# Kernel tuning notes

Measured on AMD Instinct MI355X. Metric: run time of the kernel, lower is better.

The kernel has to match this reference:

```python
import jax, jax.numpy as jnp
import numpy as np

N_NODES = 100000
N_EDGES = 1600000
HID = 128


def setup_inputs() -> dict:
    key = jax.random.key(0)
    ks = jax.random.split(key, 16)

    def w(k, fan_in, fan_out, scale=None):
        s = scale if scale is not None else 1.0 / np.sqrt(fan_in)
        return (jax.random.normal(k, (fan_in, fan_out), jnp.float32) * s)

    inp = {
        "h": jax.random.normal(ks[0], (N_NODES, HID), jnp.float32),
        "edge_index": jax.random.randint(ks[1], (2, N_EDGES), 0, N_NODES, jnp.int64),
        "x": jax.random.normal(ks[2], (N_NODES, 3), jnp.float32),
        "v": jax.random.normal(ks[3], (N_NODES, 3), jnp.float32),
        # edge_mlp: Linear(257,128) -> ReLU -> Linear(128,128) -> ReLU
        "we1": w(ks[4], 2 * HID + 1, HID), "be1": jnp.zeros((HID,), jnp.float32),
        "we2": w(ks[5], HID, HID), "be2": jnp.zeros((HID,), jnp.float32),
        # node_mlp: Linear(384,128) -> ReLU -> Linear(128,128)
        "wn1": w(ks[6], 3 * HID, HID), "bn1": jnp.zeros((HID,), jnp.float32),
        "wn2": w(ks[7], HID, HID), "bn2": jnp.zeros((HID,), jnp.float32),
        # coord_mlp_vel: Linear(128,128) -> ReLU -> Linear(128,1)
        "wv1": w(ks[8], HID, HID), "bv1": jnp.zeros((HID,), jnp.float32),
        "wv2": w(ks[9], HID, 1), "bv2": jnp.zeros((1,), jnp.float32),
        # coord_mlp: Linear(128,128) -> ReLU -> Linear(128,1, bias=False, xavier gain 0.001)
        "wc1": w(ks[10], HID, HID), "bc1": jnp.zeros((HID,), jnp.float32),
        "wc2": w(ks[11], HID, 1, scale=0.001),
    }
    return inp


def reference(h, edge_index, x, v, we1, be1, we2, be2, wn1, bn1, wn2, bn2,
              wv1, bv1, wv2, bv2, wc1, bc1, wc2):
    n = h.shape[0]
    row, col = edge_index[0], edge_index[1]

    # coord2radial
    coord_diff = x[row] - x[col]                                  # [M, 3]
    radial = jnp.sum(coord_diff * coord_diff, axis=1, keepdims=True)  # [M, 1]

    # edge_model (no attention, no edge_attr)
    e_in = jnp.concatenate([h[row], h[col], radial], axis=1)      # [M, 257]
    edge_feat = jax.nn.relu(jax.nn.relu(e_in @ we1 + be1) @ we2 + be2)  # [M, 128]

    # coord_model: per-edge scalar gate, clamp, segment-mean over row
    gate = jax.nn.relu(edge_feat @ wc1 + bc1) @ wc2               # [M, 1]
    trans = jnp.clip(coord_diff * gate, -100.0, 100.0)            # [M, 3]
    num = jax.ops.segment_sum(trans, row, num_segments=n)         # [N, 3]
    cnt = jax.ops.segment_sum(jnp.ones_like(trans), row, num_segments=n)
    f = (num / jnp.maximum(cnt, 1.0)) * 1.0                       # coords_weight = 1.0

    # update: v' = gate(h) * v + f ; x' = x + v'
    vel_gate = jax.nn.relu(h @ wv1 + bv1) @ wv2 + bv2             # [N, 1]
    v_new = vel_gate * v + f
    x_new = x + v_new

    # node_model with others=h: cat[h, h, segment_sum(edge_feat)]
    agg = jax.ops.segment_sum(edge_feat, row, num_segments=n)     # [N, 128]
    n_in = jnp.concatenate([h, h, agg], axis=1)                   # [N, 384]
    h_new = h + (jax.nn.relu(n_in @ wn1 + bn1) @ wn2 + bn2)       # recurrent residual

    return h_new, x_new, v_new
```

## Files before the change

### kernel.cpp

```cpp
#include <hip/hip_runtime.h>
#include <hip/hip_bf16.h>
#include <stdint.h>

typedef __bf16 bf16_t;
typedef __bf16 bf16x8 __attribute__((ext_vector_type(8)));
typedef float f32x4 __attribute__((ext_vector_type(4)));

#define HID 128

__device__ __forceinline__ bf16_t* swz(bf16_t* base, int row, int rowBytes, int byteInRow) {
    return (bf16_t*)((char*)base + row * rowBytes + (byteInRow ^ ((row & 7) << 4)));
}
__device__ __forceinline__ const bf16_t* swzc(const bf16_t* base, int row, int rowBytes, int byteInRow) {
    return (const bf16_t*)((const char*)base + row * rowBytes + (byteInRow ^ ((row & 7) << 4)));
}

__device__ __forceinline__ bf16x8 pack8(float4 a, float4 b) {
    bf16x8 r;
    r[0] = (bf16_t)a.x; r[1] = (bf16_t)a.y; r[2] = (bf16_t)a.z; r[3] = (bf16_t)a.w;
    r[4] = (bf16_t)b.x; r[5] = (bf16_t)b.y; r[6] = (bf16_t)b.z; r[7] = (bf16_t)b.w;
    return r;
}

__device__ __forceinline__ bool is_i64(const int* ei) {
    return ((ei[1] | ei[3] | ei[5] | ei[7]) == 0);
}
__device__ __forceinline__ int eidx(const int* __restrict__ ei, int i, bool i64) {
    return i64 ? ei[2 * i] : ei[i];
}

__global__ void prep_kernel(const float* __restrict__ we1, const float* __restrict__ we2,
                            const float* __restrict__ wc1, const float* __restrict__ wn1,
                            const float* __restrict__ wn2, const float* __restrict__ wv1,
                            bf16_t* w1t, float* w1last, bf16_t* w2t, bf16_t* wc1t,
                            bf16_t* wn1t, bf16_t* wn2t, bf16_t* wv1t) {
    int idx = blockIdx.x * 256 + threadIdx.x;
    if (idx < 32768) { int j = idx >> 8, k = idx & 255; w1t[idx] = (bf16_t)we1[k * 128 + j]; return; }
    idx -= 32768;
    if (idx < 128) { w1last[idx] = we1[256 * 128 + idx]; return; }
    idx -= 128;
    if (idx < 16384) { int j = idx >> 7, k = idx & 127; w2t[idx] = (bf16_t)we2[k * 128 + j]; return; }
    idx -= 16384;
    if (idx < 16384) { int j = idx >> 7, k = idx & 127; wc1t[idx] = (bf16_t)wc1[k * 128 + j]; return; }
    idx -= 16384;
    if (idx < 32768) {
        int j = idx >> 8, k = idx & 255;
        float val = (k < 128) ? (wn1[k * 128 + j] + wn1[(k + 128) * 128 + j])
                              : wn1[(k + 128) * 128 + j];
        wn1t[idx] = (bf16_t)val; return;
    }
    idx -= 32768;
    if (idx < 16384) { int j = idx >> 7, k = idx & 127; wn2t[idx] = (bf16_t)wn2[k * 128 + j]; return; }
    idx -= 16384;
    if (idx < 16384) { int j = idx >> 7, k = idx & 127; wv1t[idx] = (bf16_t)wv1[k * 128 + j]; return; }
}

__global__ void hist_kernel(const int* __restrict__ ei, int* __restrict__ hist, int M) {
    const bool i64 = is_i64(ei);
    int e = blockIdx.x * 256 + threadIdx.x;
    if (e < M) atomicAdd(&hist[eidx(ei, e, i64)], 1);
}

#define NCHUNK 128
__global__ void scanA_kernel(const int* __restrict__ hist, int* __restrict__ chunk_sums,
                             int N, int CHUNK) {
    __shared__ int red[256];
    int b = blockIdx.x, tid = threadIdx.x;
    int lo = b * CHUNK, hi = min(N, lo + CHUNK);
    int s = 0;
    for (int i = lo + tid; i < hi; i += 256) s += hist[i];
    red[tid] = s; __syncthreads();
    for (int ofs = 128; ofs > 0; ofs >>= 1) {
        if (tid < ofs) red[tid] += red[tid + ofs];
        __syncthreads();
    }
    if (tid == 0) chunk_sums[b] = red[0];
}

__global__ void scanB_kernel(const int* __restrict__ chunk_sums, int* __restrict__ chunk_base,
                             int* __restrict__ off, int N, int M) {
    __shared__ int s[NCHUNK];
    int tid = threadIdx.x;
    if (tid < NCHUNK) s[tid] = chunk_sums[tid];
    __syncthreads();
    if (tid == 0) {
        int run = 0;
        for (int i = 0; i < NCHUNK; i++) { int v = s[i]; s[i] = run; run += v; }
        off[N] = M;
    }
    __syncthreads();
    if (tid < NCHUNK) chunk_base[tid] = s[tid];
}

__global__ void scanC_kernel(const int* __restrict__ hist, const int* __restrict__ chunk_base,
                             int* __restrict__ off, int* __restrict__ cursor, int N, int CHUNK) {
    __shared__ int sd[256];
    int b = blockIdx.x, tid = threadIdx.x;
    int carry = chunk_base[b];
    for (int base = 0; base < CHUNK; base += 256) {
        int li = base + tid;
        int i = b * CHUNK + li;
        int v = (li < CHUNK && i < N) ? hist[i] : 0;
        sd[tid] = v; __syncthreads();
        for (int ofs = 1; ofs < 256; ofs <<= 1) {
            int t = (tid >= ofs) ? sd[tid - ofs] : 0;
            __syncthreads();
            sd[tid] += t;
            __syncthreads();
        }
        int excl = sd[tid] - v;
        if (li < CHUNK && i < N) { off[i] = carry + excl; cursor[i] = carry + excl; }
        carry += sd[255];
        __syncthreads();
    }
}

__global__ void scatter_kernel(const int* __restrict__ ei, int* __restrict__ cursor,
                               int* __restrict__ sorted_eid, int* __restrict__ sorted_row, int M) {
    const bool i64 = is_i64(ei);
    int e = blockIdx.x * 256 + threadIdx.x;
    if (e < M) {
        int r = eidx(ei, e, i64);
        int p = atomicAdd(&cursor[r], 1);
        sorted_eid[p] = e;
        sorted_row[p] = r;
    }
}

__global__ __launch_bounds__(512, 2) void edge_kernel(
    const float* __restrict__ h, const int* __restrict__ ei, const float* __restrict__ x,
    const float* __restrict__ be1, const float* __restrict__ be2,
    const float* __restrict__ bc1, const float* __restrict__ wc2,
    const bf16_t* __restrict__ w1t, const float* __restrict__ w1last,
    const bf16_t* __restrict__ w2t, const bf16_t* __restrict__ wc1t,
    const int* __restrict__ sorted_eid, const int* __restrict__ sorted_row,
    float* __restrict__ agg, float* __restrict__ num,
    int M, int N) {
    __shared__ bf16_t lw1[128 * 256];
    __shared__ bf16_t lw2[128 * 128];
    __shared__ bf16_t lbuf[8][2][16 * 128];

    const int tid = threadIdx.x;
    for (int c = tid; c < 4096; c += 512) {
        int row = c >> 5, cin = c & 31;
        float4 d4 = ((const float4*)w1t)[c];
        *(float4*)swz(lw1, row, 512, cin * 16) = d4;
    }
    for (int c = tid; c < 2048; c += 512) {
        int row = c >> 4, cin = c & 15;
        float4 d4 = ((const float4*)w2t)[c];
        *(float4*)swz(lw2, row, 256, cin * 16) = d4;
    }
    __syncthreads();

    const bool i64 = is_i64(ei);
    const int wave = tid >> 6, lane = tid & 63;
    const int l15 = lane & 15, l4 = lane >> 4;
    bf16_t* b0 = lbuf[wave][0];
    bf16_t* b1 = lbuf[wave][1];
    const int wid = blockIdx.x * 8 + wave;
    const int stride = gridDim.x * 8;
    const int ntiles = M >> 4;

    for (int t = wid; t < ntiles; t += stride) {
        const int e0 = t << 4;
        const int s = lane >> 2, p = lane & 3;
        const int er = sorted_row[e0 + s];
        const int eid = sorted_eid[e0 + s];
        const int ec = eidx(ei, M + eid, i64);
        const float* hr = h + (size_t)er * HID + p * 32;
        const float* hc = h + (size_t)ec * HID + p * 32;
#pragma unroll
        for (int c2 = 0; c2 < 4; c2++) {
            float4 a = *(const float4*)(hr + c2 * 8);
            float4 b = *(const float4*)(hr + c2 * 8 + 4);
            *(bf16x8*)swz(b0, s, 256, (p * 4 + c2) * 16) = pack8(a, b);
        }
#pragma unroll
        for (int c2 = 0; c2 < 4; c2++) {
            float4 a = *(const float4*)(hc + c2 * 8);
            float4 b = *(const float4*)(hc + c2 * 8 + 4);
            *(bf16x8*)swz(b1, s, 256, (p * 4 + c2) * 16) = pack8(a, b);
        }
        float d0 = x[er * 3 + 0] - x[ec * 3 + 0];
        float d1 = x[er * 3 + 1] - x[ec * 3 + 1];
        float d2 = x[er * 3 + 2] - x[ec * 3 + 2];
        float radial = d0 * d0 + d1 * d1 + d2 * d2;
        __builtin_amdgcn_wave_barrier();

        float rad4[4];
#pragma unroll
        for (int r = 0; r < 4; r++) rad4[r] = __shfl(radial, (l4 * 4 + r) * 4, 64);

        f32x4 acc[8];
#pragma unroll
        for (int n = 0; n < 8; n++) {
            int j = n * 16 + l15;
            float bb = be1[j], wl = w1last[j];
#pragma unroll
            for (int r = 0; r < 4; r++) acc[n][r] = bb + rad4[r] * wl;
        }
#pragma unroll
        for (int kk = 0; kk < 8; kk++) {
            const bf16_t* ab = (kk < 4) ? b0 : b1;
            bf16x8 af = *(const bf16x8*)swzc(ab, l15, 256, (kk & 3) * 64 + l4 * 16);
#pragma unroll
            for (int n = 0; n < 8; n++) {
                bf16x8 bf = *(const bf16x8*)swzc(lw1, n * 16 + l15, 512, kk * 64 + l4 * 16);
                acc[n] = __builtin_amdgcn_mfma_f32_16x16x32_bf16(af, bf, acc[n], 0, 0, 0);
            }
        }
#pragma unroll
        for (int n = 0; n < 8; n++) {
#pragma unroll
            for (int r = 0; r < 4; r++) {
                int rw = l4 * 4 + r;
                *swz(b0, rw, 256, (n * 16 + l15) * 2) = (bf16_t)fmaxf(acc[n][r], 0.f);
            }
        }
        __builtin_amdgcn_wave_barrier();

        f32x4 acc2[8];
#pragma unroll
        for (int n = 0; n < 8; n++) {
            float bb = be2[n * 16 + l15];
#pragma unroll
            for (int r = 0; r < 4; r++) acc2[n][r] = bb;
        }
#pragma unroll
        for (int kk = 0; kk < 4; kk++) {
            bf16x8 af = *(const bf16x8*)swzc(b0, l15, 256, kk * 64 + l4 * 16);
#pragma unroll
            for (int n = 0; n < 8; n++) {
                bf16x8 bf = *(const bf16x8*)swzc(lw2, n * 16 + l15, 256, kk * 64 + l4 * 16);
                acc2[n] = __builtin_amdgcn_mfma_f32_16x16x32_bf16(af, bf, acc2[n], 0, 0, 0);
            }
        }
#pragma unroll
        for (int n = 0; n < 8; n++) {
#pragma unroll
            for (int r = 0; r < 4; r++) {
                float v_ = fmaxf(acc2[n][r], 0.f);
                int rw = l4 * 4 + r;
                *swz(b1, rw, 256, (n * 16 + l15) * 2) = (bf16_t)v_;
            }
        }
        __builtin_amdgcn_wave_barrier();

        f32x4 acc3[8];
#pragma unroll
        for (int n = 0; n < 8; n++) {
            float bb = bc1[n * 16 + l15];
#pragma unroll
            for (int r = 0; r < 4; r++) acc3[n][r] = bb;
        }
#pragma unroll
        for (int kk = 0; kk < 4; kk++) {
            bf16x8 af = *(const bf16x8*)swzc(b1, l15, 256, kk * 64 + l4 * 16);
#pragma unroll
            for (int n = 0; n < 8; n++) {
                bf16x8 bf = *(const bf16x8*)(wc1t + (n * 16 + l15) * 128 + kk * 32 + l4 * 8);
                acc3[n] = __builtin_amdgcn_mfma_f32_16x16x32_bf16(af, bf, acc3[n], 0, 0, 0);
            }
        }
        float pr[4] = {0.f, 0.f, 0.f, 0.f};
#pragma unroll
        for (int n = 0; n < 8; n++) {
            float w = wc2[n * 16 + l15];
#pragma unroll
            for (int r = 0; r < 4; r++) pr[r] += fmaxf(acc3[n][r], 0.f) * w;
        }
#pragma unroll
        for (int m = 1; m < 16; m <<= 1) {
#pragma unroll
            for (int r = 0; r < 4; r++) pr[r] += __shfl_xor(pr[r], m, 16);
        }

        {
            int s3 = s & 3;
            float g = (s3 == 0) ? pr[0] : ((s3 == 1) ? pr[1] : ((s3 == 2) ? pr[2] : pr[3]));
            if ((lane & 3) == 0) {
                float t0 = fminf(fmaxf(d0 * g, -100.f), 100.f);
                float t1 = fminf(fmaxf(d1 * g, -100.f), 100.f);
                float t2 = fminf(fmaxf(d2 * g, -100.f), 100.f);
                atomicAdd(num + (size_t)er * 3 + 0, t0);
                atomicAdd(num + (size_t)er * 3 + 1, t1);
                atomicAdd(num + (size_t)er * 3 + 2, t2);
            }
        }

        int er16[16];
#pragma unroll
        for (int rw = 0; rw < 16; rw++) er16[rw] = __shfl(er, rw * 4, 64);

        const int c0 = lane, c1 = lane + 64;
        float s0 = 0.f, s1 = 0.f;
        int prev = er16[0];
#pragma unroll
        for (int rw = 0; rw < 16; rw++) {
            if (rw > 0 && er16[rw] != prev) {
                atomicAdd(agg + (size_t)prev * HID + c0, s0);
                atomicAdd(agg + (size_t)prev * HID + c1, s1);
                s0 = 0.f; s1 = 0.f;
                prev = er16[rw];
            }
            s0 += (float)*swzc(b1, rw, 256, c0 * 2);
            s1 += (float)*swzc(b1, rw, 256, c1 * 2);
        }
        atomicAdd(agg + (size_t)prev * HID + c0, s0);
        atomicAdd(agg + (size_t)prev * HID + c1, s1);
        __builtin_amdgcn_wave_barrier();
    }
}

__global__ __launch_bounds__(256, 1) void node_kernel(
    const float* __restrict__ h, const float* __restrict__ x, const float* __restrict__ v,
    const float* __restrict__ bn1, const float* __restrict__ bn2,
    const float* __restrict__ bv1, const float* __restrict__ bv2,
    const float* __restrict__ wv2,
    const bf16_t* __restrict__ wn1t, const bf16_t* __restrict__ wn2t,
    const bf16_t* __restrict__ wv1t,
    const float* __restrict__ num, const int* __restrict__ off,
    float* __restrict__ out_h, float* __restrict__ out_x, float* __restrict__ out_v,
    int N) {
    __shared__ bf16_t lw1[128 * 256];
    __shared__ bf16_t lw2[128 * 128];
    __shared__ bf16_t lbuf[4][3][16 * 128];

    const int tid = threadIdx.x;
    for (int c = tid; c < 4096; c += 256) {
        int row = c >> 5, cin = c & 31;
        *(float4*)swz(lw1, row, 512, cin * 16) = ((const float4*)wn1t)[c];
    }
    for (int c = tid; c < 2048; c += 256) {
        int row = c >> 4, cin = c & 15;
        *(float4*)swz(lw2, row, 256, cin * 16) = ((const float4*)wn2t)[c];
    }
    __syncthreads();

    const int wave = tid >> 6, lane = tid & 63;
    const int l15 = lane & 15, l4 = lane >> 4;
    bf16_t* b0 = lbuf[wave][0];
    bf16_t* b1 = lbuf[wave][1];
    bf16_t* b2 = lbuf[wave][2];
    const int wid = blockIdx.x * 4 + wave;
    const int stride = gridDim.x * 4;
    const int nt = N >> 4;

    for (int t = wid; t < nt; t += stride) {
        const int m0 = t << 4;
        const int s = lane >> 2, p = lane & 3;
        const float* hp = h + (size_t)(m0 + s) * HID + p * 32;
        const float* ap = out_h + (size_t)(m0 + s) * HID + p * 32;
#pragma unroll
        for (int c2 = 0; c2 < 4; c2++) {
            float4 a = *(const float4*)(hp + c2 * 8);
            float4 b = *(const float4*)(hp + c2 * 8 + 4);
            *(bf16x8*)swz(b0, s, 256, (p * 4 + c2) * 16) = pack8(a, b);
        }
#pragma unroll
        for (int c2 = 0; c2 < 4; c2++) {
            float fa[8];
            *(float4*)fa = *(const float4*)(ap + c2 * 8);
            *(float4*)(fa + 4) = *(const float4*)(ap + c2 * 8 + 4);
            bf16x8 hi8, lo8;
#pragma unroll
            for (int i = 0; i < 8; i++) {
                bf16_t hi = (bf16_t)fa[i];
                hi8[i] = hi;
                lo8[i] = (bf16_t)(fa[i] - (float)hi);
            }
            *(bf16x8*)swz(b1, s, 256, (p * 4 + c2) * 16) = hi8;
            *(bf16x8*)swz(b2, s, 256, (p * 4 + c2) * 16) = lo8;
        }
        __builtin_amdgcn_wave_barrier();

        f32x4 av[8];
#pragma unroll
        for (int n = 0; n < 8; n++) {
            float bb = bv1[n * 16 + l15];
#pragma unroll
            for (int r = 0; r < 4; r++) av[n][r] = bb;
        }
#pragma unroll
        for (int kk = 0; kk < 4; kk++) {
            bf16x8 af = *(const bf16x8*)swzc(b0, l15, 256, kk * 64 + l4 * 16);
#pragma unroll
            for (int n = 0; n < 8; n++) {
                bf16x8 bf = *(const bf16x8*)(wv1t + (n * 16 + l15) * 128 + kk * 32 + l4 * 8);
                av[n] = __builtin_amdgcn_mfma_f32_16x16x32_bf16(af, bf, av[n], 0, 0, 0);
            }
        }
        float pv[4] = {0.f, 0.f, 0.f, 0.f};
#pragma unroll
        for (int n = 0; n < 8; n++) {
            float w = wv2[n * 16 + l15];
#pragma unroll
            for (int r = 0; r < 4; r++) pv[r] += fmaxf(av[n][r], 0.f) * w;
        }
#pragma unroll
        for (int m = 1; m < 16; m <<= 1) {
#pragma unroll
            for (int r = 0; r < 4; r++) pv[r] += __shfl_xor(pv[r], m, 16);
        }
        float bv2v = bv2[0];
        if (l15 == 0) {
#pragma unroll
            for (int r = 0; r < 4; r++) {
                int m = m0 + l4 * 4 + r;
                float vg = pv[r] + bv2v;
                float c = (float)(off[m + 1] - off[m]);
                float inv = 1.0f / fmaxf(c, 1.0f);
#pragma unroll
                for (int i = 0; i < 3; i++) {
                    float f = num[(size_t)m * 3 + i] * inv;
                    float vn = vg * v[(size_t)m * 3 + i] + f;
                    out_v[(size_t)m * 3 + i] = vn;
                    out_x[(size_t)m * 3 + i] = x[(size_t)m * 3 + i] + vn;
                }
            }
        }

        f32x4 a1[8];
#pragma unroll
        for (int n = 0; n < 8; n++) {
            float bb = bn1[n * 16 + l15];
#pragma unroll
            for (int r = 0; r < 4; r++) a1[n][r] = bb;
        }
#pragma unroll
        for (int kk = 0; kk < 12; kk++) {
            const bf16_t* ab = (kk < 4) ? b0 : ((kk < 8) ? b1 : b2);
            bf16x8 af = *(const bf16x8*)swzc(ab, l15, 256, (kk & 3) * 64 + l4 * 16);
            int kb = (kk < 8) ? kk : (kk - 4);
#pragma unroll
            for (int n = 0; n < 8; n++) {
                bf16x8 bf = *(const bf16x8*)swzc(lw1, n * 16 + l15, 512, kb * 64 + l4 * 16);
                a1[n] = __builtin_amdgcn_mfma_f32_16x16x32_bf16(af, bf, a1[n], 0, 0, 0);
            }
        }
#pragma unroll
        for (int n = 0; n < 8; n++) {
#pragma unroll
            for (int r = 0; r < 4; r++) {
                int rw = l4 * 4 + r;
                *swz(b0, rw, 256, (n * 16 + l15) * 2) = (bf16_t)fmaxf(a1[n][r], 0.f);
            }
        }
        __builtin_amdgcn_wave_barrier();

        f32x4 a2[8];
#pragma unroll
        for (int n = 0; n < 8; n++) {
            float bb = bn2[n * 16 + l15];
#pragma unroll
            for (int r = 0; r < 4; r++) a2[n][r] = bb;
        }
#pragma unroll
        for (int kk = 0; kk < 4; kk++) {
            bf16x8 af = *(const bf16x8*)swzc(b0, l15, 256, kk * 64 + l4 * 16);
#pragma unroll
            for (int n = 0; n < 8; n++) {
                bf16x8 bf = *(const bf16x8*)swzc(lw2, n * 16 + l15, 256, kk * 64 + l4 * 16);
                a2[n] = __builtin_amdgcn_mfma_f32_16x16x32_bf16(af, bf, a2[n], 0, 0, 0);
            }
        }
#pragma unroll
        for (int n = 0; n < 8; n++) {
            int j = n * 16 + l15;
#pragma unroll
            for (int r = 0; r < 4; r++) {
                int m = m0 + l4 * 4 + r;
                out_h[(size_t)m * HID + j] = h[(size_t)m * HID + j] + a2[n][r];
            }
        }
    }
}

extern "C" void kernel_launch(void* const* d_in, const int* in_sizes, int n_in,
                              void* d_out, int out_size, void* d_ws, size_t ws_size,
                              hipStream_t stream) {
    const float* h   = (const float*)d_in[0];
    const int*   ei  = (const int*)d_in[1];
    const float* x   = (const float*)d_in[2];
    const float* v   = (const float*)d_in[3];
    const float* we1 = (const float*)d_in[4];
    const float* be1 = (const float*)d_in[5];
    const float* we2 = (const float*)d_in[6];
    const float* be2 = (const float*)d_in[7];
    const float* wn1 = (const float*)d_in[8];
    const float* bn1 = (const float*)d_in[9];
    const float* wn2 = (const float*)d_in[10];
    const float* bn2 = (const float*)d_in[11];
    const float* wv1 = (const float*)d_in[12];
    const float* bv1 = (const float*)d_in[13];
    const float* wv2 = (const float*)d_in[14];
    const float* bv2 = (const float*)d_in[15];
    const float* wc1 = (const float*)d_in[16];
    const float* bc1 = (const float*)d_in[17];
    const float* wc2 = (const float*)d_in[18];

    const int N = in_sizes[0] / HID;
    const int M = in_sizes[1] / 2;

    float* out_h = (float*)d_out;
    float* out_x = out_h + (size_t)N * HID;
    float* out_v = out_x + (size_t)N * 3;

    char* ws = (char*)d_ws;
    auto align256 = [](size_t v) { return (v + 255) & ~(size_t)255; };
    size_t o = 0;
    bf16_t* w1t    = (bf16_t*)(ws + o); o += 65536;
    float*  w1last = (float*)(ws + o);  o += 512;
    bf16_t* w2t    = (bf16_t*)(ws + o); o += 32768;
    bf16_t* wc1t   = (bf16_t*)(ws + o); o += 32768;
    bf16_t* wn1t   = (bf16_t*)(ws + o); o += 65536;
    bf16_t* wn2t   = (bf16_t*)(ws + o); o += 32768;
    bf16_t* wv1t   = (bf16_t*)(ws + o); o += 32768;
    float*  num    = (float*)(ws + o);        o = align256(o + (size_t)N * 12);
    int*    hist   = (int*)(ws + o);          o = align256(o + (size_t)N * 4);
    int*    off    = (int*)(ws + o);          o = align256(o + (size_t)(N + 1) * 4);
    int*    cursor = (int*)(ws + o);          o = align256(o + (size_t)N * 4);
    int*    chunk_sums = (int*)(ws + o);      o = align256(o + NCHUNK * 4);
    int*    chunk_base = (int*)(ws + o);      o = align256(o + NCHUNK * 4);
    int*    sorted_eid = (int*)(ws + o);      o = align256(o + (size_t)M * 4);
    int*    sorted_row = (int*)(ws + o);      o = align256(o + (size_t)M * 4);

    const int CHUNK = (N + NCHUNK - 1) / NCHUNK;

    hipMemsetAsync(out_h, 0, (size_t)N * HID * sizeof(float), stream);
    hipMemsetAsync(num, 0, (size_t)N * 12, stream);
    hipMemsetAsync(hist, 0, (size_t)N * 4, stream);

    prep_kernel<<<513, 256, 0, stream>>>(we1, we2, wc1, wn1, wn2, wv1,
                                         w1t, w1last, w2t, wc1t, wn1t, wn2t, wv1t);
    hist_kernel<<<(M + 255) / 256, 256, 0, stream>>>(ei, hist, M);
    scanA_kernel<<<NCHUNK, 256, 0, stream>>>(hist, chunk_sums, N, CHUNK);
    scanB_kernel<<<1, 256, 0, stream>>>(chunk_sums, chunk_base, off, N, M);
    scanC_kernel<<<NCHUNK, 256, 0, stream>>>(hist, chunk_base, off, cursor, N, CHUNK);
    scatter_kernel<<<(M + 255) / 256, 256, 0, stream>>>(ei, cursor, sorted_eid, sorted_row, M);

    edge_kernel<<<256, 512, 0, stream>>>(h, ei, x, be1, be2, bc1, wc2,
                                         w1t, w1last, w2t, wc1t,
                                         sorted_eid, sorted_row,
                                         out_h, num, M, N);
    node_kernel<<<256, 256, 0, stream>>>(h, x, v, bn1, bn2, bv1, bv2, wv2,
                                         wn1t, wn2t, wv1t, num, off,
                                         out_h, out_x, out_v, N);
}
```

Baseline: 1.568 ms.

## Load MFMA A-fragments directly from global and double waves per block

Both the edge and node kernels stop staging gathered h rows (and the aggregated features) through per-wave LDS buffers. They instead load the float rows straight into registers and pack them to bf16 MFMA fragments. This halves per-wave LDS use, which lets blocks grow from 512/256 to 1024 threads (16 waves) within the same LDS budget, raising occupancy to better hide gather latency. The trade-offs are less coalesced per-lane global loads and a launch_bounds(1024,4) hint that may squeeze registers and cause spills.

```diff
diff --git a/kernel.cpp b/kernel.cpp
--- a/kernel.cpp
+++ b/kernel.cpp
@@ -127,7 +127,7 @@
     }
 }
 
-__global__ __launch_bounds__(512, 2) void edge_kernel(
+__global__ __launch_bounds__(1024, 4) void edge_kernel(
     const float* __restrict__ h, const int* __restrict__ ei, const float* __restrict__ x,
     const float* __restrict__ be1, const float* __restrict__ be2,
     const float* __restrict__ bc1, const float* __restrict__ wc2,
@@ -138,55 +138,38 @@
     int M, int N) {
     __shared__ bf16_t lw1[128 * 256];
     __shared__ bf16_t lw2[128 * 128];
-    __shared__ bf16_t lbuf[8][2][16 * 128];
+    __shared__ bf16_t lbuf[16][16 * 128];
 
     const int tid = threadIdx.x;
-    for (int c = tid; c < 4096; c += 512) {
+    for (int c = tid; c < 4096; c += 1024) {
         int row = c >> 5, cin = c & 31;
-        float4 d4 = ((const float4*)w1t)[c];
-        *(float4*)swz(lw1, row, 512, cin * 16) = d4;
-    }
-    for (int c = tid; c < 2048; c += 512) {
+        *(float4*)swz(lw1, row, 512, cin * 16) = ((const float4*)w1t)[c];
+    }
+    for (int c = tid; c < 2048; c += 1024) {
         int row = c >> 4, cin = c & 15;
-        float4 d4 = ((const float4*)w2t)[c];
-        *(float4*)swz(lw2, row, 256, cin * 16) = d4;
+        *(float4*)swz(lw2, row, 256, cin * 16) = ((const float4*)w2t)[c];
     }
     __syncthreads();
 
     const bool i64 = is_i64(ei);
     const int wave = tid >> 6, lane = tid & 63;
     const int l15 = lane & 15, l4 = lane >> 4;
-    bf16_t* b0 = lbuf[wave][0];
-    bf16_t* b1 = lbuf[wave][1];
-    const int wid = blockIdx.x * 8 + wave;
-    const int stride = gridDim.x * 8;
+    bf16_t* b0 = lbuf[wave];
+    const int wid = blockIdx.x * 16 + wave;
+    const int stride = gridDim.x * 16;
     const int ntiles = M >> 4;
 
     for (int t = wid; t < ntiles; t += stride) {
         const int e0 = t << 4;
-        const int s = lane >> 2, p = lane & 3;
-        const int er = sorted_row[e0 + s];
-        const int eid = sorted_eid[e0 + s];
-        const int ec = eidx(ei, M + eid, i64);
-        const float* hr = h + (size_t)er * HID + p * 32;
-        const float* hc = h + (size_t)ec * HID + p * 32;
-#pragma unroll
-        for (int c2 = 0; c2 < 4; c2++) {
-            float4 a = *(const float4*)(hr + c2 * 8);
-            float4 b = *(const float4*)(hr + c2 * 8 + 4);
-            *(bf16x8*)swz(b0, s, 256, (p * 4 + c2) * 16) = pack8(a, b);
-        }
-#pragma unroll
-        for (int c2 = 0; c2 < 4; c2++) {
-            float4 a = *(const float4*)(hc + c2 * 8);
-            float4 b = *(const float4*)(hc + c2 * 8 + 4);
-            *(bf16x8*)swz(b1, s, 256, (p * 4 + c2) * 16) = pack8(a, b);
-        }
-        float d0 = x[er * 3 + 0] - x[ec * 3 + 0];
-        float d1 = x[er * 3 + 1] - x[ec * 3 + 1];
-        float d2 = x[er * 3 + 2] - x[ec * 3 + 2];
+        const int erl = sorted_row[e0 + l15];
+        const int ecl = eidx(ei, M + sorted_eid[e0 + l15], i64);
+        const int s = lane >> 2;
+        const int ers = sorted_row[e0 + s];
+        const int ecs = eidx(ei, M + sorted_eid[e0 + s], i64);
+        float d0 = x[ers * 3 + 0] - x[ecs * 3 + 0];
+        float d1 = x[ers * 3 + 1] - x[ecs * 3 + 1];
+        float d2 = x[ers * 3 + 2] - x[ecs * 3 + 2];
         float radial = d0 * d0 + d1 * d1 + d2 * d2;
-        __builtin_amdgcn_wave_barrier();
 
         float rad4[4];
 #pragma unroll
@@ -200,10 +183,14 @@
 #pragma unroll
             for (int r = 0; r < 4; r++) acc[n][r] = bb + rad4[r] * wl;
         }
+        const float* hbr = h + (size_t)erl * HID;
+        const float* hbc = h + (size_t)ecl * HID;
 #pragma unroll
         for (int kk = 0; kk < 8; kk++) {
-            const bf16_t* ab = (kk < 4) ? b0 : b1;
-            bf16x8 af = *(const bf16x8*)swzc(ab, l15, 256, (kk & 3) * 64 + l4 * 16);
+            const float* ap = ((kk < 4) ? (hbr + kk * 32) : (hbc + (kk - 4) * 32)) + l4 * 8;
+            float4 a = *(const float4*)ap;
+            float4 b = *(const float4*)(ap + 4);
+            bf16x8 af = pack8(a, b);
 #pragma unroll
             for (int n = 0; n < 8; n++) {
                 bf16x8 bf = *(const bf16x8*)swzc(lw1, n * 16 + l15, 512, kk * 64 + l4 * 16);
@@ -236,13 +223,14 @@
                 acc2[n] = __builtin_amdgcn_mfma_f32_16x16x32_bf16(af, bf, acc2[n], 0, 0, 0);
             }
         }
+        __builtin_amdgcn_wave_barrier();
 #pragma unroll
         for (int n = 0; n < 8; n++) {
 #pragma unroll
             for (int r = 0; r < 4; r++) {
                 float v_ = fmaxf(acc2[n][r], 0.f);
                 int rw = l4 * 4 + r;
-                *swz(b1, rw, 256, (n * 16 + l15) * 2) = (bf16_t)v_;
+                *swz(b0, rw, 256, (n * 16 + l15) * 2) = (bf16_t)v_;
             }
         }
         __builtin_amdgcn_wave_barrier();
@@ -256,7 +244,7 @@
         }
 #pragma unroll
         for (int kk = 0; kk < 4; kk++) {
-            bf16x8 af = *(const bf16x8*)swzc(b1, l15, 256, kk * 64 + l4 * 16);
+            bf16x8 af = *(const bf16x8*)swzc(b0, l15, 256, kk * 64 + l4 * 16);
 #pragma unroll
             for (int n = 0; n < 8; n++) {
                 bf16x8 bf = *(const bf16x8*)(wc1t + (n * 16 + l15) * 128 + kk * 32 + l4 * 8);
@@ -283,15 +271,15 @@
                 float t0 = fminf(fmaxf(d0 * g, -100.f), 100.f);
                 float t1 = fminf(fmaxf(d1 * g, -100.f), 100.f);
                 float t2 = fminf(fmaxf(d2 * g, -100.f), 100.f);
-                atomicAdd(num + (size_t)er * 3 + 0, t0);
-                atomicAdd(num + (size_t)er * 3 + 1, t1);
-                atomicAdd(num + (size_t)er * 3 + 2, t2);
+                atomicAdd(num + (size_t)ers * 3 + 0, t0);
+                atomicAdd(num + (size_t)ers * 3 + 1, t1);
+                atomicAdd(num + (size_t)ers * 3 + 2, t2);
             }
         }
 
         int er16[16];
 #pragma unroll
-        for (int rw = 0; rw < 16; rw++) er16[rw] = __shfl(er, rw * 4, 64);
+        for (int rw = 0; rw < 16; rw++) er16[rw] = __shfl(erl, rw, 64);
 
         const int c0 = lane, c1 = lane + 64;
         float s0 = 0.f, s1 = 0.f;
@@ -304,8 +292,8 @@
                 s0 = 0.f; s1 = 0.f;
                 prev = er16[rw];
             }
-            s0 += (float)*swzc(b1, rw, 256, c0 * 2);
-            s1 += (float)*swzc(b1, rw, 256, c1 * 2);
+            s0 += (float)*swzc(b0, rw, 256, c0 * 2);
+            s1 += (float)*swzc(b0, rw, 256, c1 * 2);
         }
         atomicAdd(agg + (size_t)prev * HID + c0, s0);
         atomicAdd(agg + (size_t)prev * HID + c1, s1);
@@ -313,7 +301,7 @@
     }
 }
 
-__global__ __launch_bounds__(256, 1) void node_kernel(
+__global__ __launch_bounds__(1024, 4) void node_kernel(
     const float* __restrict__ h, const float* __restrict__ x, const float* __restrict__ v,
     const float* __restrict__ bn1, const float* __restrict__ bn2,
     const float* __restrict__ bv1, const float* __restrict__ bv2,
@@ -325,14 +313,14 @@
     int N) {
     __shared__ bf16_t lw1[128 * 256];
     __shared__ bf16_t lw2[128 * 128];
-    __shared__ bf16_t lbuf[4][3][16 * 128];
+    __shared__ bf16_t lbuf[16][16 * 128];
 
     const int tid = threadIdx.x;
-    for (int c = tid; c < 4096; c += 256) {
+    for (int c = tid; c < 4096; c += 1024) {
         int row = c >> 5, cin = c & 31;
         *(float4*)swz(lw1, row, 512, cin * 16) = ((const float4*)wn1t)[c];
     }
-    for (int c = tid; c < 2048; c += 256) {
+    for (int c = tid; c < 2048; c += 1024) {
         int row = c >> 4, cin = c & 15;
         *(float4*)swz(lw2, row, 256, cin * 16) = ((const float4*)wn2t)[c];
     }
@@ -340,40 +328,15 @@
 
     const int wave = tid >> 6, lane = tid & 63;
     const int l15 = lane & 15, l4 = lane >> 4;
-    bf16_t* b0 = lbuf[wave][0];
-    bf16_t* b1 = lbuf[wave][1];
-    bf16_t* b2 = lbuf[wave][2];
-    const int wid = blockIdx.x * 4 + wave;
-    const int stride = gridDim.x * 4;
+    bf16_t* b0 = lbuf[wave];
+    const int wid = blockIdx.x * 16 + wave;
+    const int stride = gridDim.x * 16;
     const int nt = N >> 4;
 
     for (int t = wid; t < nt; t += stride) {
         const int m0 = t << 4;
-        const int s = lane >> 2, p = lane & 3;
-        const float* hp = h + (size_t)(m0 + s) * HID + p * 32;
-        const float* ap = out_h + (size_t)(m0 + s) * HID + p * 32;
-#pragma unroll
-        for (int c2 = 0; c2 < 4; c2++) {
-            float4 a = *(const float4*)(hp + c2 * 8);
-            float4 b = *(const float4*)(hp + c2 * 8 + 4);
-            *(bf16x8*)swz(b0, s, 256, (p * 4 + c2) * 16) = pack8(a, b);
-        }
-#pragma unroll
-        for (int c2 = 0; c2 < 4; c2++) {
-            float fa[8];
-            *(float4*)fa = *(const float4*)(ap + c2 * 8);
-            *(float4*)(fa + 4) = *(const float4*)(ap + c2 * 8 + 4);
-            bf16x8 hi8, lo8;
-#pragma unroll
-            for (int i = 0; i < 8; i++) {
-                bf16_t hi = (bf16_t)fa[i];
-                hi8[i] = hi;
-                lo8[i] = (bf16_t)(fa[i] - (float)hi);
-            }
-            *(bf16x8*)swz(b1, s, 256, (p * 4 + c2) * 16) = hi8;
-            *(bf16x8*)swz(b2, s, 256, (p * 4 + c2) * 16) = lo8;
-        }
-        __builtin_amdgcn_wave_barrier();
+        const float* hb = h + (size_t)(m0 + l15) * HID;
+        const float* ab = out_h + (size_t)(m0 + l15) * HID;
 
         f32x4 av[8];
 #pragma unroll
@@ -384,7 +347,8 @@
         }
 #pragma unroll
         for (int kk = 0; kk < 4; kk++) {
-            bf16x8 af = *(const bf16x8*)swzc(b0, l15, 256, kk * 64 + l4 * 16);
+            const float* ap = hb + kk * 32 + l4 * 8;
+            bf16x8 af = pack8(*(const float4*)ap, *(const float4*)(ap + 4));
 #pragma unroll
             for (int n = 0; n < 8; n++) {
                 bf16x8 bf = *(const bf16x8*)(wv1t + (n * 16 + l15) * 128 + kk * 32 + l4 * 8);
@@ -429,14 +393,37 @@
             for (int r = 0; r < 4; r++) a1[n][r] = bb;
         }
 #pragma unroll
-        for (int kk = 0; kk < 12; kk++) {
-            const bf16_t* ab = (kk < 4) ? b0 : ((kk < 8) ? b1 : b2);
-            bf16x8 af = *(const bf16x8*)swzc(ab, l15, 256, (kk & 3) * 64 + l4 * 16);
-            int kb = (kk < 8) ? kk : (kk - 4);
-#pragma unroll
-            for (int n = 0; n < 8; n++) {
-                bf16x8 bf = *(const bf16x8*)swzc(lw1, n * 16 + l15, 512, kb * 64 + l4 * 16);
+        for (int kk = 0; kk < 4; kk++) {
+            const float* ap = hb + kk * 32 + l4 * 8;
+            bf16x8 af = pack8(*(const float4*)ap, *(const float4*)(ap + 4));
+#pragma unroll
+            for (int n = 0; n < 8; n++) {
+                bf16x8 bf = *(const bf16x8*)swzc(lw1, n * 16 + l15, 512, kk * 64 + l4 * 16);
                 a1[n] = __builtin_amdgcn_mfma_f32_16x16x32_bf16(af, bf, a1[n], 0, 0, 0);
+            }
+        }
+#pragma unroll
+        for (int c2 = 0; c2 < 4; c2++) {
+            const float* ap = ab + c2 * 32 + l4 * 8;
+            float fa[8];
+            *(float4*)fa = *(const float4*)ap;
+            *(float4*)(fa + 4) = *(const float4*)(ap + 4);
+            bf16x8 hi8, lo8;
+#pragma unroll
+            for (int i = 0; i < 8; i++) {
+                bf16_t hi = (bf16_t)fa[i];
+                hi8[i] = hi;
+                lo8[i] = (bf16_t)(fa[i] - (float)hi);
+            }
+#pragma unroll
+            for (int n = 0; n < 8; n++) {
+                bf16x8 bfh = *(const bf16x8*)swzc(lw1, n * 16 + l15, 512, (4 + c2) * 64 + l4 * 16);
+                a1[n] = __builtin_amdgcn_mfma_f32_16x16x32_bf16(hi8, bfh, a1[n], 0, 0, 0);
+            }
+#pragma unroll
+            for (int n = 0; n < 8; n++) {
+                bf16x8 bfl = *(const bf16x8*)swzc(lw1, n * 16 + l15, 512, (4 + c2) * 64 + l4 * 16);
+                a1[n] = __builtin_amdgcn_mfma_f32_16x16x32_bf16(lo8, bfl, a1[n], 0, 0, 0);
             }
         }
 #pragma unroll
@@ -474,6 +461,7 @@
                 out_h[(size_t)m * HID + j] = h[(size_t)m * HID + j] + a2[n][r];
             }
         }
+        __builtin_amdgcn_wave_barrier();
     }
 }
 
@@ -540,11 +528,11 @@
     scanC_kernel<<<NCHUNK, 256, 0, stream>>>(hist, chunk_base, off, cursor, N, CHUNK);
     scatter_kernel<<<(M + 255) / 256, 256, 0, stream>>>(ei, cursor, sorted_eid, sorted_row, M);
 
-    edge_kernel<<<256, 512, 0, stream>>>(h, ei, x, be1, be2, bc1, wc2,
-                                         w1t, w1last, w2t, wc1t,
-                                         sorted_eid, sorted_row,
-                                         out_h, num, M, N);
-    node_kernel<<<256, 256, 0, stream>>>(h, x, v, bn1, bn2, bv1, bv2, wv2,
-                                         wn1t, wn2t, wv1t, num, off,
-                                         out_h, out_x, out_v, N);
-}
+    edge_kernel<<<256, 1024, 0, stream>>>(h, ei, x, be1, be2, bc1, wc2,
+                                          w1t, w1last, w2t, wc1t,
+                                          sorted_eid, sorted_row,
+                                          out_h, num, M, N);
+    node_kernel<<<256, 1024, 0, stream>>>(h, x, v, bn1, bn2, bv1, bv2, wv2,
+                                          wn1t, wn2t, wv1t, num, off,
+                                          out_h, out_x, out_v, N);
+}
```

Result: slower. 2.342 ms (+49.3%).

## Give edge waves contiguous tile ranges with carried segment sums; restructure node kernel

Applied to the files above, without the earlier changes.

The edge kernel now assigns each wave a contiguous block of sorted edge tiles and carries the per-row partial sum across tiles, so a row segment spanning tiles is flushed with one atomic instead of several. The node kernel drops the per-wave LDS staging of h and agg, building MFMA A-operands directly from global loads in registers, and launches 1024-thread blocks with 16 waves. This is meant to cut atomic traffic and LDS round trips and raise node-kernel occupancy, at the cost of redundant global reads of h and heavier register pressure under the 1024-thread launch bound.

```diff
diff --git a/kernel.cpp b/kernel.cpp
--- a/kernel.cpp
+++ b/kernel.cpp
@@ -143,13 +143,11 @@
     const int tid = threadIdx.x;
     for (int c = tid; c < 4096; c += 512) {
         int row = c >> 5, cin = c & 31;
-        float4 d4 = ((const float4*)w1t)[c];
-        *(float4*)swz(lw1, row, 512, cin * 16) = d4;
+        *(float4*)swz(lw1, row, 512, cin * 16) = ((const float4*)w1t)[c];
     }
     for (int c = tid; c < 2048; c += 512) {
         int row = c >> 4, cin = c & 15;
-        float4 d4 = ((const float4*)w2t)[c];
-        *(float4*)swz(lw2, row, 256, cin * 16) = d4;
+        *(float4*)swz(lw2, row, 256, cin * 16) = ((const float4*)w2t)[c];
     }
     __syncthreads();
 
@@ -159,10 +157,17 @@
     bf16_t* b0 = lbuf[wave][0];
     bf16_t* b1 = lbuf[wave][1];
     const int wid = blockIdx.x * 8 + wave;
-    const int stride = gridDim.x * 8;
+    const int nw = gridDim.x * 8;
     const int ntiles = M >> 4;
-
-    for (int t = wid; t < ntiles; t += stride) {
+    const int K = (ntiles + nw - 1) / nw;
+    const int tb = wid * K;
+    const int te = min(ntiles, tb + K);
+
+    const int c0 = lane, c1 = lane + 64;
+    int carryRow = -1;
+    float cs0 = 0.f, cs1 = 0.f;
+
+    for (int t = tb; t < te; t++) {
         const int e0 = t << 4;
         const int s = lane >> 2, p = lane & 3;
         const int er = sorted_row[e0 + s];
@@ -293,27 +298,28 @@
 #pragma unroll
         for (int rw = 0; rw < 16; rw++) er16[rw] = __shfl(er, rw * 4, 64);
 
-        const int c0 = lane, c1 = lane + 64;
-        float s0 = 0.f, s1 = 0.f;
-        int prev = er16[0];
 #pragma unroll
         for (int rw = 0; rw < 16; rw++) {
-            if (rw > 0 && er16[rw] != prev) {
-                atomicAdd(agg + (size_t)prev * HID + c0, s0);
-                atomicAdd(agg + (size_t)prev * HID + c1, s1);
-                s0 = 0.f; s1 = 0.f;
-                prev = er16[rw];
-            }
-            s0 += (float)*swzc(b1, rw, 256, c0 * 2);
-            s1 += (float)*swzc(b1, rw, 256, c1 * 2);
-        }
-        atomicAdd(agg + (size_t)prev * HID + c0, s0);
-        atomicAdd(agg + (size_t)prev * HID + c1, s1);
+            int r = er16[rw];
+            if (r != carryRow) {
+                if (carryRow >= 0) {
+                    atomicAdd(agg + (size_t)carryRow * HID + c0, cs0);
+                    atomicAdd(agg + (size_t)carryRow * HID + c1, cs1);
+                }
+                carryRow = r; cs0 = 0.f; cs1 = 0.f;
+            }
+            cs0 += (float)*swzc(b1, rw, 256, c0 * 2);
+            cs1 += (float)*swzc(b1, rw, 256, c1 * 2);
+        }
         __builtin_amdgcn_wave_barrier();
     }
-}
-
-__global__ __launch_bounds__(256, 1) void node_kernel(
+    if (carryRow >= 0) {
+        atomicAdd(agg + (size_t)carryRow * HID + c0, cs0);
+        atomicAdd(agg + (size_t)carryRow * HID + c1, cs1);
+    }
+}
+
+__global__ __launch_bounds__(1024, 4) void node_kernel(
     const float* __restrict__ h, const float* __restrict__ x, const float* __restrict__ v,
     const float* __restrict__ bn1, const float* __restrict__ bn2,
     const float* __restrict__ bv1, const float* __restrict__ bv2,
@@ -325,14 +331,14 @@
     int N) {
     __shared__ bf16_t lw1[128 * 256];
     __shared__ bf16_t lw2[128 * 128];
-    __shared__ bf16_t lbuf[4][3][16 * 128];
+    __shared__ bf16_t lbuf[16][16 * 128];
 
     const int tid = threadIdx.x;
-    for (int c = tid; c < 4096; c += 256) {
+    for (int c = tid; c < 4096; c += 1024) {
         int row = c >> 5, cin = c & 31;
         *(float4*)swz(lw1, row, 512, cin * 16) = ((const float4*)wn1t)[c];
     }
-    for (int c = tid; c < 2048; c += 256) {
+    for (int c = tid; c < 2048; c += 1024) {
         int row = c >> 4, cin = c & 15;
         *(float4*)swz(lw2, row, 256, cin * 16) = ((const float4*)wn2t)[c];
     }
@@ -340,40 +346,15 @@
 
     const int wave = tid >> 6, lane = tid & 63;
     const int l15 = lane & 15, l4 = lane >> 4;
-    bf16_t* b0 = lbuf[wave][0];
-    bf16_t* b1 = lbuf[wave][1];
-    bf16_t* b2 = lbuf[wave][2];
-    const int wid = blockIdx.x * 4 + wave;
-    const int stride = gridDim.x * 4;
+    bf16_t* b0 = lbuf[wave];
+    const int wid = blockIdx.x * 16 + wave;
+    const int stride = gridDim.x * 16;
     const int nt = N >> 4;
 
     for (int t = wid; t < nt; t += stride) {
         const int m0 = t << 4;
-        const int s = lane >> 2, p = lane & 3;
-        const float* hp = h + (size_t)(m0 + s) * HID + p * 32;
-        const float* ap = out_h + (size_t)(m0 + s) * HID + p * 32;
-#pragma unroll
-        for (int c2 = 0; c2 < 4; c2++) {
-            float4 a = *(const float4*)(hp + c2 * 8);
-            float4 b = *(const float4*)(hp + c2 * 8 + 4);
-            *(bf16x8*)swz(b0, s, 256, (p * 4 + c2) * 16) = pack8(a, b);
-        }
-#pragma unroll
-        for (int c2 = 0; c2 < 4; c2++) {
-            float fa[8];
-            *(float4*)fa = *(const float4*)(ap + c2 * 8);
-            *(float4*)(fa + 4) = *(const float4*)(ap + c2 * 8 + 4);
-            bf16x8 hi8, lo8;
-#pragma unroll
-            for (int i = 0; i < 8; i++) {
-                bf16_t hi = (bf16_t)fa[i];
-                hi8[i] = hi;
-                lo8[i] = (bf16_t)(fa[i] - (float)hi);
-            }
-            *(bf16x8*)swz(b1, s, 256, (p * 4 + c2) * 16) = hi8;
-            *(bf16x8*)swz(b2, s, 256, (p * 4 + c2) * 16) = lo8;
-        }
-        __builtin_amdgcn_wave_barrier();
+        const float* hb = h + (size_t)(m0 + l15) * HID;
+        const float* ab = out_h + (size_t)(m0 + l15) * HID;
 
         f32x4 av[8];
 #pragma unroll
@@ -384,7 +365,8 @@
         }
 #pragma unroll
         for (int kk = 0; kk < 4; kk++) {
-            bf16x8 af = *(const bf16x8*)swzc(b0, l15, 256, kk * 64 + l4 * 16);
+            const float* ap = hb + kk * 32 + l4 * 8;
+            bf16x8 af = pack8(*(const float4*)ap, *(const float4*)(ap + 4));
 #pragma unroll
             for (int n = 0; n < 8; n++) {
                 bf16x8 bf = *(const bf16x8*)(wv1t + (n * 16 + l15) * 128 + kk * 32 + l4 * 8);
@@ -429,14 +411,37 @@
             for (int r = 0; r < 4; r++) a1[n][r] = bb;
         }
 #pragma unroll
-        for (int kk = 0; kk < 12; kk++) {
-            const bf16_t* ab = (kk < 4) ? b0 : ((kk < 8) ? b1 : b2);
-            bf16x8 af = *(const bf16x8*)swzc(ab, l15, 256, (kk & 3) * 64 + l4 * 16);
-            int kb = (kk < 8) ? kk : (kk - 4);
-#pragma unroll
-            for (int n = 0; n < 8; n++) {
-                bf16x8 bf = *(const bf16x8*)swzc(lw1, n * 16 + l15, 512, kb * 64 + l4 * 16);
+        for (int kk = 0; kk < 4; kk++) {
+            const float* ap = hb + kk * 32 + l4 * 8;
+            bf16x8 af = pack8(*(const float4*)ap, *(const float4*)(ap + 4));
+#pragma unroll
+            for (int n = 0; n < 8; n++) {
+                bf16x8 bf = *(const bf16x8*)swzc(lw1, n * 16 + l15, 512, kk * 64 + l4 * 16);
                 a1[n] = __builtin_amdgcn_mfma_f32_16x16x32_bf16(af, bf, a1[n], 0, 0, 0);
+            }
+        }
+#pragma unroll
+        for (int c2 = 0; c2 < 4; c2++) {
+            const float* ap = ab + c2 * 32 + l4 * 8;
+            float fa[8];
+            *(float4*)fa = *(const float4*)ap;
+            *(float4*)(fa + 4) = *(const float4*)(ap + 4);
+            bf16x8 hi8, lo8;
+#pragma unroll
+            for (int i = 0; i < 8; i++) {
+                bf16_t hi = (bf16_t)fa[i];
+                hi8[i] = hi;
+                lo8[i] = (bf16_t)(fa[i] - (float)hi);
+            }
+#pragma unroll
+            for (int n = 0; n < 8; n++) {
+                bf16x8 bfh = *(const bf16x8*)swzc(lw1, n * 16 + l15, 512, (4 + c2) * 64 + l4 * 16);
+                a1[n] = __builtin_amdgcn_mfma_f32_16x16x32_bf16(hi8, bfh, a1[n], 0, 0, 0);
+            }
+#pragma unroll
+            for (int n = 0; n < 8; n++) {
+                bf16x8 bfl = *(const bf16x8*)swzc(lw1, n * 16 + l15, 512, (4 + c2) * 64 + l4 * 16);
+                a1[n] = __builtin_amdgcn_mfma_f32_16x16x32_bf16(lo8, bfl, a1[n], 0, 0, 0);
             }
         }
 #pragma unroll
@@ -474,6 +479,7 @@
                 out_h[(size_t)m * HID + j] = h[(size_t)m * HID + j] + a2[n][r];
             }
         }
+        __builtin_amdgcn_wave_barrier();
     }
 }
 
@@ -544,7 +550,7 @@
                                          w1t, w1last, w2t, wc1t,
                                          sorted_eid, sorted_row,
                                          out_h, num, M, N);
-    node_kernel<<<256, 256, 0, stream>>>(h, x, v, bn1, bn2, bv1, bv2, wv2,
-                                         wn1t, wn2t, wv1t, num, off,
-                                         out_h, out_x, out_v, N);
-}
+    node_kernel<<<256, 1024, 0, stream>>>(h, x, v, bn1, bn2, bv1, bv2, wv2,
+                                          wn1t, wn2t, wv1t, num, off,
+                                          out_h, out_x, out_v, N);
+}
```

Measured after the change: 1.597 ms. No clear change (+1.8%).
